# Kernel optimization log

Measured on AMD Instinct MI355X. Metric: run time of the kernel, lower is better.

The kernel has to match this reference:

```python
import jax, jax.numpy as jnp
import numpy as np

MAX_REL = 30  # hardcoded in SpatialVelocityCrossAttention (rel_pos_enc max_rel_pos=30)
N_HEADS = 8


def conv1d_same(x, w, b):
    # x: [B, L, Cin], w: [O, I, K] (torch layout), b: [O]; 'same' padding for odd K
    k = w.shape[-1]
    y = jax.lax.conv_general_dilated(
        x, jnp.transpose(w, (2, 1, 0)), (1,), [(k // 2, k // 2)],
        dimension_numbers=('NHC', 'HIO', 'NHC'))
    return y + b


def rel_pos_enc(xm, emb, dw_w, dw_b):
    # Faithful closed form of RelativePositionalEncoding.forward.
    # fused[b,i,j] = xm[b,j] + emb[clip(j-i,-R,R)+R]; depthwise 3-tap conv along j per row i;
    # output[b,j] = mean_i( conv_out if i==j else fused ) =
    #   xm[b,j] + (sum_i pos[i,j] - (xm[b,j]+emb[R]) + diag_conv[b,j]) / S
    B, S, D = xm.shape
    r = jnp.arange(S)
    idx = jnp.clip(r[None, :] - r[:, None], -MAX_REL, MAX_REL) + MAX_REL  # [i, j]
    counts = (idx[:, :, None] == jnp.arange(2 * MAX_REL + 1)[None, None, :]).sum(0)  # [j, 2R+1]
    pos_sum = counts.astype(xm.dtype) @ emb  # [S, D] = sum_i emb[clip(j-i)+R]
    fC = xm + emb[MAX_REL]                      # fused[b,j,j]
    # padded-conv neighbors of the diagonal (zero input outside sequence):
    fL = jnp.pad(xm[:, :-1] + emb[MAX_REL - 1], ((0, 0), (1, 0), (0, 0)))  # fused[b,j,j-1]
    fR = jnp.pad(xm[:, 1:] + emb[MAX_REL + 1], ((0, 0), (0, 1), (0, 0)))   # fused[b,j,j+1]
    diag_conv = fL * dw_w[:, 0] + fC * dw_w[:, 1] + fR * dw_w[:, 2] + dw_b
    return xm + (pos_sum[None] - fC + diag_conv) / S


def setup_inputs() -> dict:
    key = jax.random.key(0)
    ks = jax.random.split(key, 16)
    B, L, MN = 32, 1024, 512           # L == 2*MN (required by Gamma.repeat(1,2,1))
    sd, vd, dm = 256, 64, 256          # spatial_dim == d_model (residual add), velocity_dim
    d3 = 3 * vd

    def w(k, shape, s=0.05):
        return jax.random.normal(k, shape, jnp.float32) * s

    return {
        'x_spatial': jax.random.normal(ks[0], (B, L, sd), jnp.float32),
        'x_velocity': jax.random.normal(ks[1], (B, MN, vd), jnp.float32),
        'Wg': w(ks[2], (dm, vd)),                 # conv_gamma (1x1, no bias)
        'ms_w3': w(ks[3], (vd, vd, 3)), 'ms_b3': jnp.zeros((vd,), jnp.float32),
        'ms_w5': w(ks[4], (vd, vd, 5)), 'ms_b5': jnp.zeros((vd,), jnp.float32),
        'ms_w7': w(ks[5], (vd, vd, 7)), 'ms_b7': jnp.zeros((vd,), jnp.float32),
        'rel_emb': w(ks[6], (2 * MAX_REL + 1, d3)),
        'dw_w': w(ks[7], (d3, 3), 0.1), 'dw_b': jnp.zeros((d3,), jnp.float32),
        'Wq': w(ks[8], (dm, sd)),
        'Wk': w(ks[9], (dm, d3)),
        'Wv': w(ks[10], (dm, d3)),
        'fc_w': w(ks[11], (dm, dm)), 'fc_b': jnp.zeros((dm,), jnp.float32),
        'ln_w': jnp.ones((dm,), jnp.float32), 'ln_b': jnp.zeros((dm,), jnp.float32),
    }


def reference(x_spatial, x_velocity, Wg, ms_w3, ms_b3, ms_w5, ms_b5, ms_w7, ms_b7,
              rel_emb, dw_w, dw_b, Wq, Wk, Wv, fc_w, fc_b, ln_w, ln_b):
    B, L, sd = x_spatial.shape
    _, MN, vd = x_velocity.shape
    dm = Wq.shape[0]
    H, dk = N_HEADS, Wq.shape[0] // N_HEADS

    # sigmoid-gated 1x1 conv on velocity
    Gamma = jax.nn.sigmoid(jnp.einsum('bsc,dc->bsd', x_velocity, Wg))  # [B, MN, dm]

    # multi-scale convs, concat on channel -> [B, MN, 3*vd]
    xm = jnp.concatenate([
        conv1d_same(x_velocity, ms_w3, ms_b3),
        conv1d_same(x_velocity, ms_w5, ms_b5),
        conv1d_same(x_velocity, ms_w7, ms_b7)], axis=-1)

    x_v_pe = rel_pos_enc(xm, rel_emb, dw_w, dw_b)  # [B, MN, 3*vd]

    # 1x1-conv Q/K/V projections, split heads channel-major (matches torch view)
    Q = jnp.einsum('blc,dc->bld', x_spatial, Wq).reshape(B, L, H, dk).transpose(0, 2, 1, 3)
    K = jnp.einsum('bsc,dc->bsd', x_v_pe, Wk).reshape(B, MN, H, dk).transpose(0, 2, 1, 3)
    V = jnp.einsum('bsc,dc->bsd', x_v_pe, Wv).reshape(B, MN, H, dk).transpose(0, 2, 1, 3)

    attn = jax.nn.softmax(jnp.einsum('bhld,bhsd->bhls', Q, K) / np.sqrt(dk).astype(np.float32), axis=-1)
    out = jnp.einsum('bhls,bhsd->bhld', attn, V)           # [B, H, L, dk]
    out = out.transpose(0, 2, 1, 3).reshape(B, L, dm)       # concat heads
    out = out @ fc_w.T + fc_b

    out = jnp.tile(Gamma, (1, 2, 1)) * out                  # Gamma.repeat(1,2,1) gating
    x = x_spatial + out
    mu = x.mean(-1, keepdims=True)
    var = x.var(-1, keepdims=True)
    return (x - mu) / jnp.sqrt(var + 1e-5) * ln_w + ln_b
```

## Files before the change

### kernel.cpp

```cpp
#include <hip/hip_runtime.h>

#define B   32
#define L   1024
#define MN  512
#define SD  256
#define VD  64
#define DM  256
#define D3  192
#define NH  8
#define DK  32
#define RMAX 30
#define NREL 61
#define SPAD 518

typedef __attribute__((ext_vector_type(8))) __bf16 bf16x8;
typedef __attribute__((ext_vector_type(4))) float  f32x4;

static __device__ __forceinline__ ushort f2bf(float f) {
  unsigned u = __float_as_uint(f);
  unsigned r = (u + 0x7FFFu + ((u >> 16) & 1u)) >> 16;
  return (ushort)r;
}
static __device__ __forceinline__ bf16x8 ldbf8(const ushort* p) {
  return __builtin_bit_cast(bf16x8, *(const uint4*)p);
}
static __device__ __forceinline__ float fexp2(float x) {
  return __builtin_amdgcn_exp2f(x);
}

__global__ __launch_bounds__(256) void prep_kernel(
    const float* __restrict__ Wg, ushort* __restrict__ Wgb,
    const float* __restrict__ Wq, ushort* __restrict__ Wqb,
    const float* __restrict__ Wk, ushort* __restrict__ Wkb,
    const float* __restrict__ Wv, ushort* __restrict__ Wvb,
    const float* __restrict__ fcw, ushort* __restrict__ fcwb,
    const float* __restrict__ xv, ushort* __restrict__ xp,
    const float* __restrict__ w3, const float* __restrict__ w5,
    const float* __restrict__ w7, ushort* __restrict__ wb,
    const float* __restrict__ emb, float* __restrict__ psum) {
  int blk = blockIdx.x;
  if (blk < 240) {
    const float* s; ushort* d; int base;
    if (blk < 16)       { s = Wg;  d = Wgb;  base = blk; }
    else if (blk < 80)  { s = Wq;  d = Wqb;  base = blk - 16; }
    else if (blk < 128) { s = Wk;  d = Wkb;  base = blk - 80; }
    else if (blk < 176) { s = Wv;  d = Wvb;  base = blk - 128; }
    else                { s = fcw; d = fcwb; base = blk - 176; }
    int i = (base * 256 + threadIdx.x) * 4;
    float4 v = *(const float4*)(s + i);
    *(ushort4*)(d + i) = make_ushort4(f2bf(v.x), f2bf(v.y), f2bf(v.z), f2bf(v.w));
  } else if (blk < 240 + 4144) {
    int i = (blk - 240) * 256 + threadIdx.x;
    if (i < B * SPAD * VD) {
      int c = i & 63;
      int bp = i >> 6;
      int b_ = bp / SPAD, p = bp - b_ * SPAD;
      int s = p - 3;
      float v = (s >= 0 && s < MN) ? xv[((size_t)b_ * MN + s) * VD + c] : 0.f;
      ushort hi = f2bf(v);
      float vh = __uint_as_float((uint)hi << 16);
      ushort lo = f2bf(v - vh);
      xp[i] = hi;
      xp[(size_t)B * SPAD * VD + i] = lo;
    }
  } else if (blk < 240 + 4144 + 192) {
    const int o = blk - (240 + 4144);
    const int scale = o >> 6, oo = o & 63;
    for (int j = threadIdx.x; j < 448; j += 256) {
      const int k7 = j >> 6, i = j & 63;
      float v = 0.f;
      if (scale == 0) {
        int k = k7 - 2; if (k >= 0 && k < 3) v = w3[((size_t)oo * VD + i) * 3 + k];
      } else if (scale == 1) {
        int k = k7 - 1; if (k >= 0 && k < 5) v = w5[((size_t)oo * VD + i) * 5 + k];
      } else {
        v = w7[((size_t)oo * VD + i) * 7 + k7];
      }
      wb[(size_t)o * 448 + j] = f2bf(v);
    }
  } else {
    const int j = blk - (240 + 4144 + 192);
    const int d = threadIdx.x;
    if (d < D3) {
      float acc = 0.f;
      for (int r = 0; r < NREL; ++r) {
        int v = r - RMAX;
        int cnt;
        if (r == 0)             cnt = max(0, MN - (j + RMAX));
        else if (r == NREL - 1) cnt = max(0, j - RMAX + 1);
        else                    cnt = (j - v >= 0 && j - v < MN) ? 1 : 0;
        acc += (float)cnt * emb[(size_t)r * D3 + d];
      }
      psum[(size_t)j * D3 + d] = acc;
    }
  }
}

template<int CIN, int OMODE, int ACT, int AF32>
static __device__ __forceinline__ void proj_body(
    int blk, const void* __restrict__ Xv, const ushort* __restrict__ Wb,
    void* __restrict__ Yv, int tid) {
  const int wave = tid >> 6, lane = tid & 63;
  const int q15 = lane & 15, quad = lane >> 4;
  const int row0 = blk * 64 + wave * 16;
  constexpr int KS = CIN / 32;

  f32x4 acc[16];
#pragma unroll
  for (int t = 0; t < 16; ++t) acc[t] = (f32x4){0.f, 0.f, 0.f, 0.f};

  const ushort* abase = (const ushort*)Xv + (size_t)(row0 + q15) * CIN + quad * 8;
  const float*  fbase = (const float*)Xv + (size_t)(row0 + q15) * CIN + quad * 8;
  const ushort* bbase = Wb + (size_t)q15 * CIN + quad * 8;
#pragma unroll 2
  for (int ks = 0; ks < KS; ++ks) {
    bf16x8 af;
    if constexpr (AF32) {
      float4 u0 = *(const float4*)(fbase + ks * 32);
      float4 u1 = *(const float4*)(fbase + ks * 32 + 4);
      uint4 p;
      p.x = (uint)f2bf(u0.x) | ((uint)f2bf(u0.y) << 16);
      p.y = (uint)f2bf(u0.z) | ((uint)f2bf(u0.w) << 16);
      p.z = (uint)f2bf(u1.x) | ((uint)f2bf(u1.y) << 16);
      p.w = (uint)f2bf(u1.z) | ((uint)f2bf(u1.w) << 16);
      af = __builtin_bit_cast(bf16x8, p);
    } else {
      af = ldbf8(abase + ks * 32);
    }
#pragma unroll
    for (int t = 0; t < 16; ++t) {
      bf16x8 bf = ldbf8(bbase + (size_t)t * 16 * CIN + ks * 32);
      acc[t] = __builtin_amdgcn_mfma_f32_16x16x32_bf16(af, bf, acc[t], 0, 0, 0);
    }
  }
#pragma unroll
  for (int reg = 0; reg < 4; ++reg) {
    const int row = row0 + quad * 4 + reg;
#pragma unroll
    for (int t = 0; t < 16; ++t) {
      int col = t * 16 + q15;
      float v = acc[t][reg];
      if (ACT == 1) v = 1.f / (1.f + __expf(-v));
      if (OMODE == 0) {
        ((float*)Yv)[(size_t)row * DM + col] = v;
      } else if (OMODE == 2) {
        int b_ = row >> 9, s = row & 511;
        int h = t >> 1, dk = (t & 1) * 16 + q15;
        ((ushort*)Yv)[((size_t)((b_ * NH + h) * DK + dk)) * MN + s] = f2bf(v);
      } else if (OMODE == 3) {
        int b_ = row >> 9, s = row & 511;
        int h = col >> 5, dk = col & 31;
        ((ushort*)Yv)[((size_t)((b_ * NH + h) * MN + s)) * DK + dk] = f2bf(v);
      } else {
        int b_ = row >> 10, q = row & 1023;
        int h = col >> 5, dk = col & 31;
        ((ushort*)Yv)[((size_t)((b_ * NH + h) * L + q)) * DK + dk] = f2bf(v);
      }
    }
  }
}

__global__ __launch_bounds__(256, 2) void proj_all_kernel(
    const float* __restrict__ xv, const ushort* __restrict__ Wgb,
    float* __restrict__ Gamma,
    const float* __restrict__ xs, const ushort* __restrict__ Wqb,
    ushort* __restrict__ Qb,
    const ushort* __restrict__ xpeb, const ushort* __restrict__ Wkb,
    ushort* __restrict__ Kp, const ushort* __restrict__ Wvb,
    ushort* __restrict__ Vt) {
  const int blk = blockIdx.x;
  const int tid = threadIdx.x;
  if (blk < 256) {
    proj_body<VD, 0, 1, 1>(blk, xv, Wgb, Gamma, tid);
  } else if (blk < 768) {
    proj_body<SD, 4, 0, 1>(blk - 256, xs, Wqb, Qb, tid);
  } else if (blk < 1024) {
    proj_body<D3, 3, 0, 0>(blk - 768, xpeb, Wkb, Kp, tid);
  } else {
    proj_body<D3, 2, 0, 0>(blk - 1024, xpeb, Wvb, Vt, tid);
  }
}

__global__ __launch_bounds__(256, 4) void conv_mfma_kernel(
    const ushort* __restrict__ Xp, const ushort* __restrict__ Wb,
    const float* __restrict__ b3, const float* __restrict__ b5,
    const float* __restrict__ b7, float* __restrict__ xm) {
  const int tid = threadIdx.x;
  const int wave = tid >> 6, lane = tid & 63;
  const int q15 = lane & 15, quad = lane >> 4;
  const int row0 = blockIdx.x * 16;
  const int b_ = row0 >> 9, s0 = row0 & 511;

  f32x4 acc[3];
#pragma unroll
  for (int t = 0; t < 3; ++t) acc[t] = (f32x4){0.f, 0.f, 0.f, 0.f};

  const ushort* hbase = Xp + ((size_t)b_ * SPAD + s0 + q15) * VD + quad * 8;
  const ushort* lbase = hbase + (size_t)B * SPAD * VD;
  const ushort* wbase = Wb + ((size_t)wave * 48 + q15) * 448 + quad * 8;

#pragma unroll 2
  for (int ks = 0; ks < 14; ++ks) {
    bf16x8 ah = ldbf8(hbase + ks * 32);
    bf16x8 al = ldbf8(lbase + ks * 32);
#pragma unroll
    for (int t = 0; t < 3; ++t) {
      bf16x8 bf = ldbf8(wbase + (size_t)t * 16 * 448 + ks * 32);
      acc[t] = __builtin_amdgcn_mfma_f32_16x16x32_bf16(ah, bf, acc[t], 0, 0, 0);
      acc[t] = __builtin_amdgcn_mfma_f32_16x16x32_bf16(al, bf, acc[t], 0, 0, 0);
    }
  }
#pragma unroll
  for (int t = 0; t < 3; ++t) {
    const int col = (wave * 3 + t) * 16 + q15;
    const float bias = col < 64 ? b3[col] : (col < 128 ? b5[col - 64] : b7[col - 128]);
#pragma unroll
    for (int reg = 0; reg < 4; ++reg) {
      const int row = row0 + quad * 4 + reg;
      xm[(size_t)row * D3 + col] = acc[t][reg] + bias;
    }
  }
}

__global__ __launch_bounds__(256) void pe4_kernel(
    const float* __restrict__ xm, const float* __restrict__ psum,
    const float* __restrict__ emb, const float* __restrict__ dww,
    const float* __restrict__ dwb, ushort* __restrict__ xpe) {
  int i = blockIdx.x * 256 + threadIdx.x;
  int d4 = (i % 48) * 4;
  int bj = i / 48;
  int j = bj & 511;
  const size_t base = (size_t)bj * D3 + d4;
  f32x4 xc = *(const f32x4*)(xm + base);
  f32x4 eC = *(const f32x4*)(emb + (size_t)RMAX * D3 + d4);
  f32x4 eL = *(const f32x4*)(emb + (size_t)(RMAX - 1) * D3 + d4);
  f32x4 eR = *(const f32x4*)(emb + (size_t)(RMAX + 1) * D3 + d4);
  f32x4 ps = *(const f32x4*)(psum + (size_t)j * D3 + d4);
  f32x4 xl = (j > 0)      ? *(const f32x4*)(xm + base - D3) : (f32x4){0.f, 0.f, 0.f, 0.f};
  f32x4 xr = (j < MN - 1) ? *(const f32x4*)(xm + base + D3) : (f32x4){0.f, 0.f, 0.f, 0.f};
  ushort4 o;
  ushort* op = (ushort*)&o;
#pragma unroll
  for (int k = 0; k < 4; ++k) {
    int d = d4 + k;
    float fC = xc[k] + eC[k];
    float fL = (j > 0)      ? xl[k] + eL[k] : 0.f;
    float fR = (j < MN - 1) ? xr[k] + eR[k] : 0.f;
    float dc = fL * dww[d * 3 + 0] + fC * dww[d * 3 + 1] + fR * dww[d * 3 + 2] + dwb[d];
    op[k] = f2bf(xc[k] + (ps[k] - fC + dc) * (1.f / MN));
  }
  *(ushort4*)(xpe + base) = o;
}

#define PSTRIDE 36
__global__ __launch_bounds__(256, 3) void attn_mfma_kernel(
    const ushort* __restrict__ Qb, const ushort* __restrict__ Kb,
    const ushort* __restrict__ Vt, ushort* __restrict__ Ao) {
  const int blk = blockIdx.x;
  const int bh = blk & 255;
  const int qc = blk >> 8;
  const int h  = bh & 7;
  const int b_ = bh >> 3;
  const int tid = threadIdx.x;
  const int wave = tid >> 6, lane = tid & 63;
  const int q15 = lane & 15, quad = lane >> 4;
  const int q0 = qc * 128 + wave * 32;

  __shared__ ushort Plds[4][2][16][PSTRIDE];
  ushort* prowA = &Plds[wave][0][q15][0];
  ushort* prowB = &Plds[wave][1][q15][0];

  const ushort* qrow = Qb + ((size_t)((b_ * NH + h) * L) + q0 + q15) * DK + quad * 8;
  const bf16x8 qfA = ldbf8(qrow);
  const bf16x8 qfB = ldbf8(qrow + (size_t)16 * DK);

  f32x4 o0A = {0.f, 0.f, 0.f, 0.f}, o1A = {0.f, 0.f, 0.f, 0.f};
  f32x4 o0B = {0.f, 0.f, 0.f, 0.f}, o1B = {0.f, 0.f, 0.f, 0.f};
  float mA = -1e30f, lA = 0.f, mB = -1e30f, lB = 0.f;
  const float sc2 = 0.17677669529663687f * 1.4426950408889634f;

  const ushort* kbase = Kb + (((size_t)(b_ * NH + h) * MN) + q15) * DK + quad * 8;
  const ushort* vbase = Vt + ((size_t)((b_ * NH + h) * DK) + q15) * MN;

#pragma unroll
  for (int c = 0; c < 4; ++c) {
    const int kb0 = c * 128;
    bf16x8 av[8];
#pragma unroll
    for (int g = 0; g < 4; ++g) {
      av[g * 2]     = ldbf8(vbase + (size_t)(kb0 + g * 32 + quad * 8));
      av[g * 2 + 1] = ldbf8(vbase + (size_t)16 * MN + (kb0 + g * 32 + quad * 8));
    }
    f32x4 sA[8], sB[8];
#pragma unroll
    for (int t = 0; t < 8; ++t) {
      bf16x8 af = ldbf8(kbase + (size_t)(kb0 + t * 16) * DK);
      f32x4 z = {0.f, 0.f, 0.f, 0.f};
      sA[t] = __builtin_amdgcn_mfma_f32_16x16x32_bf16(af, qfA, z, 0, 0, 0);
      sB[t] = __builtin_amdgcn_mfma_f32_16x16x32_bf16(af, qfB, z, 0, 0, 0);
    }
    float mlA = -1e30f, mlB = -1e30f;
#pragma unroll
    for (int t = 0; t < 8; ++t)
#pragma unroll
      for (int r = 0; r < 4; ++r) {
        sA[t][r] *= sc2; mlA = fmaxf(mlA, sA[t][r]);
        sB[t][r] *= sc2; mlB = fmaxf(mlB, sB[t][r]);
      }
    mlA = fmaxf(mlA, __shfl_xor(mlA, 16));
    mlB = fmaxf(mlB, __shfl_xor(mlB, 16));
    mlA = fmaxf(mlA, __shfl_xor(mlA, 32));
    mlB = fmaxf(mlB, __shfl_xor(mlB, 32));
    float mnA = fmaxf(mA, mlA), mnB = fmaxf(mB, mlB);
    float aA = fexp2(mA - mnA), aB = fexp2(mB - mnB);
    mA = mnA; mB = mnB;
    lA *= aA; lB *= aB;
#pragma unroll
    for (int r = 0; r < 4; ++r) {
      o0A[r] *= aA; o1A[r] *= aA;
      o0B[r] *= aB; o1B[r] *= aB;
    }
#pragma unroll
    for (int g = 0; g < 4; ++g) {
#pragma unroll
      for (int tp = 0; tp < 2; ++tp) {
        int t = 2 * g + tp;
        float a0 = fexp2(sA[t][0] - mA), a1 = fexp2(sA[t][1] - mA);
        float a2 = fexp2(sA[t][2] - mA), a3 = fexp2(sA[t][3] - mA);
        lA += (a0 + a1) + (a2 + a3);
        uint uA01 = __builtin_amdgcn_perm(__float_as_uint(a1), __float_as_uint(a0), 0x07060302u);
        uint uA23 = __builtin_amdgcn_perm(__float_as_uint(a3), __float_as_uint(a2), 0x07060302u);
        *(uint2*)(prowA + tp * 16 + quad * 4) = make_uint2(uA01, uA23);
        float b0 = fexp2(sB[t][0] - mB), b1 = fexp2(sB[t][1] - mB);
        float b2 = fexp2(sB[t][2] - mB), b3 = fexp2(sB[t][3] - mB);
        lB += (b0 + b1) + (b2 + b3);
        uint uB01 = __builtin_amdgcn_perm(__float_as_uint(b1), __float_as_uint(b0), 0x07060302u);
        uint uB23 = __builtin_amdgcn_perm(__float_as_uint(b3), __float_as_uint(b2), 0x07060302u);
        *(uint2*)(prowB + tp * 16 + quad * 4) = make_uint2(uB01, uB23);
      }
      bf16x8 bfA = ldbf8(prowA + quad * 8);
      bf16x8 bfB = ldbf8(prowB + quad * 8);
      o0A = __builtin_amdgcn_mfma_f32_16x16x32_bf16(av[g * 2],     bfA, o0A, 0, 0, 0);
      o1A = __builtin_amdgcn_mfma_f32_16x16x32_bf16(av[g * 2 + 1], bfA, o1A, 0, 0, 0);
      o0B = __builtin_amdgcn_mfma_f32_16x16x32_bf16(av[g * 2],     bfB, o0B, 0, 0, 0);
      o1B = __builtin_amdgcn_mfma_f32_16x16x32_bf16(av[g * 2 + 1], bfB, o1B, 0, 0, 0);
    }
  }
  lA += __shfl_xor(lA, 16); lA += __shfl_xor(lA, 32);
  lB += __shfl_xor(lB, 16); lB += __shfl_xor(lB, 32);
  float rA = 1.f / lA, rB = 1.f / lB;
  ushort* obA = Ao + ((size_t)((b_ * NH + h) * L) + q0 + q15) * DK + quad * 4;
  *(ushort4*)(obA)      = make_ushort4(f2bf(o0A[0] * rA), f2bf(o0A[1] * rA),
                                       f2bf(o0A[2] * rA), f2bf(o0A[3] * rA));
  *(ushort4*)(obA + 16) = make_ushort4(f2bf(o1A[0] * rA), f2bf(o1A[1] * rA),
                                       f2bf(o1A[2] * rA), f2bf(o1A[3] * rA));
  ushort* obB = obA + (size_t)16 * DK;
  *(ushort4*)(obB)      = make_ushort4(f2bf(o0B[0] * rB), f2bf(o0B[1] * rB),
                                       f2bf(o0B[2] * rB), f2bf(o0B[3] * rB));
  *(ushort4*)(obB + 16) = make_ushort4(f2bf(o1B[0] * rB), f2bf(o1B[1] * rB),
                                       f2bf(o1B[2] * rB), f2bf(o1B[3] * rB));
}

__global__ __launch_bounds__(256, 2) void final_mfma_kernel(
    const ushort* __restrict__ Ao, const ushort* __restrict__ fcwb,
    const float* __restrict__ fcb, const float* __restrict__ G,
    const float* __restrict__ Xs, const float* __restrict__ lnw,
    const float* __restrict__ lnb, float* __restrict__ out) {
  const int tid = threadIdx.x;
  const int wave = tid >> 6, lane = tid & 63;
  const int q15 = lane & 15, quad = lane >> 4;
  const int row0 = blockIdx.x * 64 + wave * 16;
  const int brow = row0 >> 10;
  const int srow = (row0 & 1023) + q15;

  f32x4 acc[16];
#pragma unroll
  for (int t = 0; t < 16; ++t) acc[t] = (f32x4){0.f, 0.f, 0.f, 0.f};

  const ushort* abase = Ao + ((size_t)(brow * NH) * L + srow) * DK + quad * 8;
  const ushort* bbase = fcwb + (size_t)q15 * DM + quad * 8;
#pragma unroll 2
  for (int ks = 0; ks < 8; ++ks) {
    bf16x8 af = ldbf8(abase + (size_t)ks * L * DK);
#pragma unroll
    for (int t = 0; t < 16; ++t) {
      bf16x8 bf = ldbf8(bbase + (size_t)t * 16 * DM + ks * 32);
      acc[t] = __builtin_amdgcn_mfma_f32_16x16x32_bf16(af, bf, acc[t], 0, 0, 0);
    }
  }
#pragma unroll
  for (int reg = 0; reg < 4; ++reg) {
    const int grow = row0 + quad * 4 + reg;
    const int b_ = grow >> 10;
    const int gl = (grow & 1023) & 511;
    const float* gbase = G + ((size_t)b_ * MN + gl) * DM + q15;
    const float* xbase = Xs + (size_t)grow * SD + q15;
    float vv[16];
    float s1 = 0.f, s2 = 0.f;
#pragma unroll
    for (int t = 0; t < 16; ++t) {
      int col = t * 16 + q15;
      float fcv = acc[t][reg] + fcb[col];
      float v = xbase[t * 16] + gbase[t * 16] * fcv;
      vv[t] = v; s1 += v; s2 += v * v;
    }
    s1 += __shfl_xor(s1, 1); s2 += __shfl_xor(s2, 1);
    s1 += __shfl_xor(s1, 2); s2 += __shfl_xor(s2, 2);
    s1 += __shfl_xor(s1, 4); s2 += __shfl_xor(s2, 4);
    s1 += __shfl_xor(s1, 8); s2 += __shfl_xor(s2, 8);
    float mu = s1 * (1.f / DM);
    float var = s2 * (1.f / DM) - mu * mu;
    float rs = rsqrtf(var + 1e-5f);
    float* obase = out + (size_t)grow * DM + q15;
#pragma unroll
    for (int t = 0; t < 16; ++t) {
      int col = t * 16 + q15;
      obase[t * 16] = (vv[t] - mu) * rs * lnw[col] + lnb[col];
    }
  }
}

extern "C" void kernel_launch(void* const* d_in, const int* in_sizes, int n_in,
                              void* d_out, int out_size, void* d_ws, size_t ws_size,
                              hipStream_t stream) {
  const float* x_spatial  = (const float*)d_in[0];
  const float* x_velocity = (const float*)d_in[1];
  const float* Wg   = (const float*)d_in[2];
  const float* w3   = (const float*)d_in[3];
  const float* b3   = (const float*)d_in[4];
  const float* w5   = (const float*)d_in[5];
  const float* b5   = (const float*)d_in[6];
  const float* w7   = (const float*)d_in[7];
  const float* b7   = (const float*)d_in[8];
  const float* remb = (const float*)d_in[9];
  const float* dww  = (const float*)d_in[10];
  const float* dwb  = (const float*)d_in[11];
  const float* Wq   = (const float*)d_in[12];
  const float* Wk   = (const float*)d_in[13];
  const float* Wv   = (const float*)d_in[14];
  const float* fcw  = (const float*)d_in[15];
  const float* fcb  = (const float*)d_in[16];
  const float* lnw  = (const float*)d_in[17];
  const float* lnb  = (const float*)d_in[18];
  float* out = (float*)d_out;

  char* w8 = (char*)d_ws;
  float*  Gamma = (float*)(w8);
  float*  xm    = (float*)(w8 + 16777216);
  float*  psum  = (float*)(w8 + 29360128);
  ushort* xpeb  = (ushort*)(w8 + 29753344);
  ushort* Qb    = (ushort*)(w8 + 36044800);
  ushort* Kp    = (ushort*)(w8 + 52822016);
  ushort* Vt    = (ushort*)(w8 + 61210624);
  ushort* Ao    = (ushort*)(w8 + 69599232);
  ushort* fcwb  = (ushort*)(w8 + 86376448);
  ushort* Wgb   = (ushort*)(w8 + 105381888);
  ushort* Wqb   = (ushort*)(w8 + 105414656);
  ushort* Wkb   = (ushort*)(w8 + 105545728);
  ushort* Wvb   = (ushort*)(w8 + 105644032);
  ushort* xvp   = (ushort*)(w8 + 69599232);
  ushort* wbigb = (ushort*)(w8 + 69599232 + 4243456);

  prep_kernel<<<240 + 4144 + 192 + 512, 256, 0, stream>>>(
      Wg, Wgb, Wq, Wqb, Wk, Wkb, Wv, Wvb, fcw, fcwb,
      x_velocity, xvp, w3, w5, w7, wbigb, remb, psum);

  conv_mfma_kernel<<<B * MN / 16, 256, 0, stream>>>(xvp, wbigb, b3, b5, b7, xm);
  pe4_kernel<<<(B * MN * 48) / 256, 256, 0, stream>>>(xm, psum, remb, dww, dwb, xpeb);

  proj_all_kernel<<<1280, 256, 0, stream>>>(
      x_velocity, Wgb, Gamma, x_spatial, Wqb, Qb, xpeb, Wkb, Kp, Wvb, Vt);

  attn_mfma_kernel<<<B * NH * (L / 128), 256, 0, stream>>>(Qb, Kp, Vt, Ao);
  final_mfma_kernel<<<B * L / 64, 256, 0, stream>>>(Ao, fcwb, fcb, Gamma,
                                                    x_spatial, lnw, lnb, out);
}
```

Before: 337.6 us.

## Fuse positional encoding into K/V projection and merge conv with Gamma/Q projections

```diff
diff --git a/kernel.cpp b/kernel.cpp
--- a/kernel.cpp
+++ b/kernel.cpp
@@ -143,14 +143,6 @@
       if (ACT == 1) v = 1.f / (1.f + __expf(-v));
       if (OMODE == 0) {
         ((float*)Yv)[(size_t)row * DM + col] = v;
-      } else if (OMODE == 2) {
-        int b_ = row >> 9, s = row & 511;
-        int h = t >> 1, dk = (t & 1) * 16 + q15;
-        ((ushort*)Yv)[((size_t)((b_ * NH + h) * DK + dk)) * MN + s] = f2bf(v);
-      } else if (OMODE == 3) {
-        int b_ = row >> 9, s = row & 511;
-        int h = col >> 5, dk = col & 31;
-        ((ushort*)Yv)[((size_t)((b_ * NH + h) * MN + s)) * DK + dk] = f2bf(v);
       } else {
         int b_ = row >> 10, q = row & 1023;
         int h = col >> 5, dk = col & 31;
@@ -160,96 +152,151 @@
   }
 }
 
-__global__ __launch_bounds__(256, 2) void proj_all_kernel(
+static __device__ __forceinline__ void conv_body(
+    int blk, const ushort* __restrict__ Xp, const ushort* __restrict__ Wb,
+    const float* __restrict__ b3, const float* __restrict__ b5,
+    const float* __restrict__ b7, float* __restrict__ xm, int tid) {
+  const int wave = tid >> 6, lane = tid & 63;
+  const int q15 = lane & 15, quad = lane >> 4;
+  const int row0 = blk * 32;
+  const int b_ = row0 >> 9, s0 = row0 & 511;
+
+  f32x4 acc0[3], acc1[3];
+#pragma unroll
+  for (int t = 0; t < 3; ++t) {
+    acc0[t] = (f32x4){0.f, 0.f, 0.f, 0.f};
+    acc1[t] = (f32x4){0.f, 0.f, 0.f, 0.f};
+  }
+  const ushort* h0 = Xp + ((size_t)b_ * SPAD + s0 + q15) * VD + quad * 8;
+  const ushort* h1 = h0 + 16 * VD;
+  const ushort* l0 = h0 + (size_t)B * SPAD * VD;
+  const ushort* l1 = l0 + 16 * VD;
+  const ushort* wbase = Wb + ((size_t)wave * 48 + q15) * 448 + quad * 8;
+
+#pragma unroll 2
+  for (int ks = 0; ks < 14; ++ks) {
+    bf16x8 ah0 = ldbf8(h0 + ks * 32), al0 = ldbf8(l0 + ks * 32);
+    bf16x8 ah1 = ldbf8(h1 + ks * 32), al1 = ldbf8(l1 + ks * 32);
+#pragma unroll
+    for (int t = 0; t < 3; ++t) {
+      bf16x8 bf = ldbf8(wbase + (size_t)t * 16 * 448 + ks * 32);
+      acc0[t] = __builtin_amdgcn_mfma_f32_16x16x32_bf16(ah0, bf, acc0[t], 0, 0, 0);
+      acc0[t] = __builtin_amdgcn_mfma_f32_16x16x32_bf16(al0, bf, acc0[t], 0, 0, 0);
+      acc1[t] = __builtin_amdgcn_mfma_f32_16x16x32_bf16(ah1, bf, acc1[t], 0, 0, 0);
+      acc1[t] = __builtin_amdgcn_mfma_f32_16x16x32_bf16(al1, bf, acc1[t], 0, 0, 0);
+    }
+  }
+#pragma unroll
+  for (int t = 0; t < 3; ++t) {
+    const int col = (wave * 3 + t) * 16 + q15;
+    const float bias = col < 64 ? b3[col] : (col < 128 ? b5[col - 64] : b7[col - 128]);
+#pragma unroll
+    for (int reg = 0; reg < 4; ++reg) {
+      const int row = row0 + quad * 4 + reg;
+      xm[(size_t)row * D3 + col] = acc0[t][reg] + bias;
+      xm[(size_t)(row + 16) * D3 + col] = acc1[t][reg] + bias;
+    }
+  }
+}
+
+__global__ __launch_bounds__(256, 2) void mega1_kernel(
+    const ushort* __restrict__ Xp, const ushort* __restrict__ Wbig,
+    const float* __restrict__ b3, const float* __restrict__ b5,
+    const float* __restrict__ b7, float* __restrict__ xm,
     const float* __restrict__ xv, const ushort* __restrict__ Wgb,
     float* __restrict__ Gamma,
     const float* __restrict__ xs, const ushort* __restrict__ Wqb,
-    ushort* __restrict__ Qb,
-    const ushort* __restrict__ xpeb, const ushort* __restrict__ Wkb,
-    ushort* __restrict__ Kp, const ushort* __restrict__ Wvb,
-    ushort* __restrict__ Vt) {
+    ushort* __restrict__ Qb) {
   const int blk = blockIdx.x;
   const int tid = threadIdx.x;
-  if (blk < 256) {
-    proj_body<VD, 0, 1, 1>(blk, xv, Wgb, Gamma, tid);
+  if (blk < 512) {
+    conv_body(blk, Xp, Wbig, b3, b5, b7, xm, tid);
   } else if (blk < 768) {
-    proj_body<SD, 4, 0, 1>(blk - 256, xs, Wqb, Qb, tid);
-  } else if (blk < 1024) {
-    proj_body<D3, 3, 0, 0>(blk - 768, xpeb, Wkb, Kp, tid);
+    proj_body<VD, 0, 1, 1>(blk - 512, xv, Wgb, Gamma, tid);
   } else {
-    proj_body<D3, 2, 0, 0>(blk - 1024, xpeb, Wvb, Vt, tid);
-  }
-}
-
-__global__ __launch_bounds__(256, 4) void conv_mfma_kernel(
-    const ushort* __restrict__ Xp, const ushort* __restrict__ Wb,
-    const float* __restrict__ b3, const float* __restrict__ b5,
-    const float* __restrict__ b7, float* __restrict__ xm) {
+    proj_body<SD, 4, 0, 1>(blk - 768, xs, Wqb, Qb, tid);
+  }
+}
+
+#define PPAD 200
+__global__ __launch_bounds__(256, 2) void projkv_pe_kernel(
+    const float* __restrict__ xm, const float* __restrict__ psum,
+    const float* __restrict__ emb, const float* __restrict__ dww,
+    const float* __restrict__ dwb, const ushort* __restrict__ Wkb,
+    const ushort* __restrict__ Wvb, ushort* __restrict__ Kp,
+    ushort* __restrict__ Vt) {
+  const int isV = blockIdx.x >> 8;
+  const int blk = blockIdx.x & 255;
   const int tid = threadIdx.x;
+  const int row0 = blk * 64;
+
+  __shared__ ushort pes[64][PPAD];
+
+#pragma unroll 2
+  for (int it = 0; it < 12; ++it) {
+    int f = it * 256 + tid;
+    int r = f / 48, c4 = (f % 48) * 4;
+    int grow = row0 + r;
+    int j = grow & 511;
+    const float* arow = xm + (size_t)grow * D3 + c4;
+    f32x4 xc = *(const f32x4*)(arow);
+    f32x4 xl = (j > 0)      ? *(const f32x4*)(arow - D3) : (f32x4){0.f, 0.f, 0.f, 0.f};
+    f32x4 xr = (j < MN - 1) ? *(const f32x4*)(arow + D3) : (f32x4){0.f, 0.f, 0.f, 0.f};
+    f32x4 ps = *(const f32x4*)(psum + (size_t)j * D3 + c4);
+    f32x4 eC = *(const f32x4*)(emb + (size_t)RMAX * D3 + c4);
+    f32x4 eL = *(const f32x4*)(emb + (size_t)(RMAX - 1) * D3 + c4);
+    f32x4 eR = *(const f32x4*)(emb + (size_t)(RMAX + 1) * D3 + c4);
+    ushort4 o;
+    ushort* op = (ushort*)&o;
+#pragma unroll
+    for (int k = 0; k < 4; ++k) {
+      int d = c4 + k;
+      float fC = xc[k] + eC[k];
+      float fL = (j > 0)      ? xl[k] + eL[k] : 0.f;
+      float fR = (j < MN - 1) ? xr[k] + eR[k] : 0.f;
+      float dc = fL * dww[d * 3 + 0] + fC * dww[d * 3 + 1] + fR * dww[d * 3 + 2] + dwb[d];
+      op[k] = f2bf(xc[k] + (ps[k] - fC + dc) * (1.f / MN));
+    }
+    *(ushort4*)(&pes[r][c4]) = o;
+  }
+  __syncthreads();
+
   const int wave = tid >> 6, lane = tid & 63;
   const int q15 = lane & 15, quad = lane >> 4;
-  const int row0 = blockIdx.x * 16;
-  const int b_ = row0 >> 9, s0 = row0 & 511;
-
-  f32x4 acc[3];
-#pragma unroll
-  for (int t = 0; t < 3; ++t) acc[t] = (f32x4){0.f, 0.f, 0.f, 0.f};
-
-  const ushort* hbase = Xp + ((size_t)b_ * SPAD + s0 + q15) * VD + quad * 8;
-  const ushort* lbase = hbase + (size_t)B * SPAD * VD;
-  const ushort* wbase = Wb + ((size_t)wave * 48 + q15) * 448 + quad * 8;
-
+  const int wrow0 = row0 + wave * 16;
+
+  f32x4 acc[16];
+#pragma unroll
+  for (int t = 0; t < 16; ++t) acc[t] = (f32x4){0.f, 0.f, 0.f, 0.f};
+
+  const ushort* abase = &pes[wave * 16 + q15][quad * 8];
+  const ushort* bbase = (isV ? Wvb : Wkb) + (size_t)q15 * D3 + quad * 8;
 #pragma unroll 2
-  for (int ks = 0; ks < 14; ++ks) {
-    bf16x8 ah = ldbf8(hbase + ks * 32);
-    bf16x8 al = ldbf8(lbase + ks * 32);
-#pragma unroll
-    for (int t = 0; t < 3; ++t) {
-      bf16x8 bf = ldbf8(wbase + (size_t)t * 16 * 448 + ks * 32);
-      acc[t] = __builtin_amdgcn_mfma_f32_16x16x32_bf16(ah, bf, acc[t], 0, 0, 0);
-      acc[t] = __builtin_amdgcn_mfma_f32_16x16x32_bf16(al, bf, acc[t], 0, 0, 0);
-    }
-  }
-#pragma unroll
-  for (int t = 0; t < 3; ++t) {
-    const int col = (wave * 3 + t) * 16 + q15;
-    const float bias = col < 64 ? b3[col] : (col < 128 ? b5[col - 64] : b7[col - 128]);
-#pragma unroll
-    for (int reg = 0; reg < 4; ++reg) {
-      const int row = row0 + quad * 4 + reg;
-      xm[(size_t)row * D3 + col] = acc[t][reg] + bias;
-    }
-  }
-}
-
-__global__ __launch_bounds__(256) void pe4_kernel(
-    const float* __restrict__ xm, const float* __restrict__ psum,
-    const float* __restrict__ emb, const float* __restrict__ dww,
-    const float* __restrict__ dwb, ushort* __restrict__ xpe) {
-  int i = blockIdx.x * 256 + threadIdx.x;
-  int d4 = (i % 48) * 4;
-  int bj = i / 48;
-  int j = bj & 511;
-  const size_t base = (size_t)bj * D3 + d4;
-  f32x4 xc = *(const f32x4*)(xm + base);
-  f32x4 eC = *(const f32x4*)(emb + (size_t)RMAX * D3 + d4);
-  f32x4 eL = *(const f32x4*)(emb + (size_t)(RMAX - 1) * D3 + d4);
-  f32x4 eR = *(const f32x4*)(emb + (size_t)(RMAX + 1) * D3 + d4);
-  f32x4 ps = *(const f32x4*)(psum + (size_t)j * D3 + d4);
-  f32x4 xl = (j > 0)      ? *(const f32x4*)(xm + base - D3) : (f32x4){0.f, 0.f, 0.f, 0.f};
-  f32x4 xr = (j < MN - 1) ? *(const f32x4*)(xm + base + D3) : (f32x4){0.f, 0.f, 0.f, 0.f};
-  ushort4 o;
-  ushort* op = (ushort*)&o;
-#pragma unroll
-  for (int k = 0; k < 4; ++k) {
-    int d = d4 + k;
-    float fC = xc[k] + eC[k];
-    float fL = (j > 0)      ? xl[k] + eL[k] : 0.f;
-    float fR = (j < MN - 1) ? xr[k] + eR[k] : 0.f;
-    float dc = fL * dww[d * 3 + 0] + fC * dww[d * 3 + 1] + fR * dww[d * 3 + 2] + dwb[d];
-    op[k] = f2bf(xc[k] + (ps[k] - fC + dc) * (1.f / MN));
-  }
-  *(ushort4*)(xpe + base) = o;
+  for (int ks = 0; ks < 6; ++ks) {
+    bf16x8 af = ldbf8(abase + ks * 32);
+#pragma unroll
+    for (int t = 0; t < 16; ++t) {
+      bf16x8 bf = ldbf8(bbase + (size_t)t * 16 * D3 + ks * 32);
+      acc[t] = __builtin_amdgcn_mfma_f32_16x16x32_bf16(af, bf, acc[t], 0, 0, 0);
+    }
+  }
+#pragma unroll
+  for (int reg = 0; reg < 4; ++reg) {
+    const int row = wrow0 + quad * 4 + reg;
+    const int b_ = row >> 9, s = row & 511;
+#pragma unroll
+    for (int t = 0; t < 16; ++t) {
+      int col = t * 16 + q15;
+      float v = acc[t][reg];
+      if (isV) {
+        int h = t >> 1, dk = (t & 1) * 16 + q15;
+        Vt[((size_t)((b_ * NH + h) * DK + dk)) * MN + s] = f2bf(v);
+      } else {
+        int h = col >> 5, dk = col & 31;
+        Kp[((size_t)((b_ * NH + h) * MN + s)) * DK + dk] = f2bf(v);
+      }
+    }
+  }
 }
 
 #define PSTRIDE 36
@@ -448,7 +495,6 @@
   float*  Gamma = (float*)(w8);
   float*  xm    = (float*)(w8 + 16777216);
   float*  psum  = (float*)(w8 + 29360128);
-  ushort* xpeb  = (ushort*)(w8 + 29753344);
   ushort* Qb    = (ushort*)(w8 + 36044800);
   ushort* Kp    = (ushort*)(w8 + 52822016);
   ushort* Vt    = (ushort*)(w8 + 61210624);
@@ -465,11 +511,12 @@
       Wg, Wgb, Wq, Wqb, Wk, Wkb, Wv, Wvb, fcw, fcwb,
       x_velocity, xvp, w3, w5, w7, wbigb, remb, psum);
 
-  conv_mfma_kernel<<<B * MN / 16, 256, 0, stream>>>(xvp, wbigb, b3, b5, b7, xm);
-  pe4_kernel<<<(B * MN * 48) / 256, 256, 0, stream>>>(xm, psum, remb, dww, dwb, xpeb);
-
-  proj_all_kernel<<<1280, 256, 0, stream>>>(
-      x_velocity, Wgb, Gamma, x_spatial, Wqb, Qb, xpeb, Wkb, Kp, Wvb, Vt);
+  mega1_kernel<<<1280, 256, 0, stream>>>(
+      xvp, wbigb, b3, b5, b7, xm,
+      x_velocity, Wgb, Gamma, x_spatial, Wqb, Qb);
+
+  projkv_pe_kernel<<<512, 256, 0, stream>>>(
+      xm, psum, remb, dww, dwb, Wkb, Wvb, Kp, Vt);
 
   attn_mfma_kernel<<<B * NH * (L / 128), 256, 0, stream>>>(Qb, Kp, Vt, Ao);
   final_mfma_kernel<<<B * L / 64, 256, 0, stream>>>(Ao, fcwb, fcb, Gamma,
```

After: 349.1 us. +3.4%, slower.
